# Kernel optimization log

Measured on AMD Instinct MI355X. Metric: run time of the kernel, lower is better.

## Reference

```python
import jax, jax.numpy as jnp
import numpy as np

KH, KW = 3, 3
STRIDE = 1
OUT_C = 512


def im2col(x, kh, kw, stride):
    # x: [N, C, H, W] -> col: [C*kh*kw, N*oh*ow]  (row order: C major, then kh, kw)
    N, C, H, W = x.shape
    oh = (H - kh) // stride + 1
    ow = (W - kw) // stride + 1
    rows = jnp.arange(oh)[:, None] * stride + jnp.arange(kh)[None, :]  # [oh, kh]
    cols = jnp.arange(ow)[:, None] * stride + jnp.arange(kw)[None, :]  # [ow, kw]
    # gather windows: result [N, C, oh, kh, ow, kw]
    A = x[:, :, rows[:, :, None, None], cols[None, None, :, :]]
    # permute to (C, kh, kw, N, oh, ow) then flatten, matching torch permute(1,4,5,0,2,3)
    col = jnp.transpose(A, (1, 3, 5, 0, 2, 4)).reshape(C * kh * kw, N * oh * ow)
    return col, oh, ow


def setup_inputs() -> dict:
    key = jax.random.key(0)
    k1, k2, k3 = jax.random.split(key, 3)
    N, C, H, W = 16, 256, 32, 32
    K_sel = (C * KH * KW) // 2  # 1152 rows kept by the binary mask
    x = jax.random.normal(k1, (N, C, H, W), dtype=jnp.float32)
    weight = jax.random.normal(k2, (K_sel, OUT_C), dtype=jnp.float32) * 0.02
    idx = jnp.sort(jax.random.randint(k3, (K_sel,), 0, C * KH * KW, dtype=jnp.int32))
    return {"x": x, "weight": weight, "idx": idx}


def reference(x, weight, idx):
    N = x.shape[0]
    col, oh, ow = im2col(x, KH, KW, STRIDE)          # [C*kh*kw, N*oh*ow]
    x_tile = col[idx, :].T                            # gather masked rows -> [N*oh*ow, K_sel]
    conv_out = x_tile @ weight                        # [N*oh*ow, out_c]
    conv_out = conv_out.reshape(N, oh * ow, OUT_C)
    conv_out = jnp.transpose(conv_out, (0, 2, 1)).reshape(N, OUT_C, oh, ow)
    return conv_out
```

## Files before the change

kernel.cpp:

```cpp
#include <hip/hip_runtime.h>
#include <stdint.h>

#define N_IMG   16
#define C_IN    256
#define H_IN    32
#define W_IN    32
#define OH      30
#define OW      30
#define K_SEL   1152
#define OUTC    512
#define RY_TOT  (N_IMG * OH)
#define M_HAT   (RY_TOT * 32)
#define X_ELEMS (N_IMG * C_IN * H_IN * W_IN)
#define OUT_SP  (OH * OW)
#define CHW     (C_IN * H_IN * W_IN)

#define TO      256
#define TM      64
#define NMT     (M_HAT / TM)
#define NOT     (OUTC / TO)
#define BSTR    40
#define KITER   (K_SEL / 32)

typedef float f32x4  __attribute__((ext_vector_type(4)));
typedef short bf16x8 __attribute__((ext_vector_type(8)));

__device__ __forceinline__ unsigned short f2bf(float f) {
    unsigned int u = __float_as_uint(f);
    u += 0x7FFFu + ((u >> 16) & 1u);
    return (unsigned short)(u >> 16);
}

__device__ __forceinline__ void gl_lds16(const void* g, void* lds) {
    __builtin_amdgcn_global_load_lds(
        (const __attribute__((address_space(1))) unsigned int*)g,
        (__attribute__((address_space(3))) unsigned int*)lds,
        16, 0, 0);
}

__global__ void prep_kernel(const int* __restrict__ idx, const float* __restrict__ w,
                            int* __restrict__ koff, unsigned short* __restrict__ wT) {
    __shared__ float tile[32][33];
    const int bx = blockIdx.x, by = blockIdx.y, t = threadIdx.x;

    if (by == 0) {
        int k = bx * 256 + t;
        if (k < K_SEL) {
            int v = idx[k];
            int c = v / 9, rem = v - c * 9;
            int i = rem / 3, j = rem - i * 3;
            koff[k] = c * (H_IN * W_IN) + i * W_IN + j;
        }
    }
    const int s0 = bx * 32, o0 = by * 32;
    const int oc = t & 31, sg = t >> 5;
#pragma unroll
    for (int i = 0; i < 4; ++i) {
        int sl = sg * 4 + i;
        tile[sl][oc] = w[(s0 + sl) * OUTC + o0 + oc];
    }
    __syncthreads();
    const int ol = t >> 3, sq = t & 7;
    unsigned int u0 = (unsigned int)f2bf(tile[sq * 4 + 0][ol]) |
                      ((unsigned int)f2bf(tile[sq * 4 + 1][ol]) << 16);
    unsigned int u1 = (unsigned int)f2bf(tile[sq * 4 + 2][ol]) |
                      ((unsigned int)f2bf(tile[sq * 4 + 3][ol]) << 16);
    uint2 pk; pk.x = u0; pk.y = u1;
    *reinterpret_cast<uint2*>(&wT[(size_t)(o0 + ol) * K_SEL + s0 + sq * 4]) = pk;
}

__global__ __launch_bounds__(256, 2)
void gemm_kernel(const unsigned short* __restrict__ wT, const float* __restrict__ x,
                 const int* __restrict__ koff, float* __restrict__ out) {
    __shared__ __align__(16) unsigned short As[2][TO * 32];
    __shared__ __align__(16) unsigned short Bs[2][TM * BSTR];
    __shared__ int koS[K_SEL];

    const int t    = threadIdx.x;
    const int wave = t >> 6;
    const int lane = t & 63;
    const int quad = lane >> 4;
    const int lo   = lane & 15;

    const int bid = blockIdx.x;
    const int mt  = bid % NMT;
    const int ot  = bid / NMT;
    const int oBase = ot * TO;
    const int mBase = mt * TM;

    for (int i = t; i < K_SEL; i += 256) koS[i] = koff[i];

    const int xw  = t & 31;
    const int xwc = min(xw, 29);
    int basex[2];
#pragma unroll
    for (int ry = 0; ry < 2; ++ry) {
        int ryg = mt * 2 + ry;
        int n = ryg / 30, y = ryg - n * 30;
        basex[ry] = n * CHW + y * W_IN + xwc;
    }

    const int kq4 = t >> 5;
    const int ks  = kq4 * 4;

    const int lrow = lane >> 2, csw = (lane & 3) ^ ((lrow >> 1) & 3);
    const unsigned short* wrow[4];
#pragma unroll
    for (int i = 0; i < 4; ++i)
        wrow[i] = wT + (size_t)(oBase + wave * 64 + i * 16 + lrow) * K_SEL + csw * 8;
    unsigned short* lA[2][4];
#pragma unroll
    for (int b = 0; b < 2; ++b)
#pragma unroll
        for (int i = 0; i < 4; ++i)
            lA[b][i] = &As[b][(wave * 64 + i * 16) * 32];

    const int aswz = quad ^ ((lo >> 1) & 3);
    const unsigned short* aB[2] = {
        &As[0][(wave * 64 + lo) * 32 + aswz * 8],
        &As[1][(wave * 64 + lo) * 32 + aswz * 8] };
    const unsigned short* bB[2] = {
        &Bs[0][lo * BSTR + quad * 8],
        &Bs[1][lo * BSTR + quad * 8] };
    unsigned short* bW[2] = {
        &Bs[0][xw * BSTR + ks],
        &Bs[1][xw * BSTR + ks] };

    __syncthreads();

    f32x4 acc[4][4] = {};
    float v[2][2][4];

    {
        int4 k4 = *(const int4*)&koS[ks];
#pragma unroll
        for (int ry = 0; ry < 2; ++ry)
#pragma unroll
            for (int j = 0; j < 4; ++j)
                v[0][ry][j] = x[basex[ry] + ((const int*)&k4)[j]];
    }
    asm volatile("s_waitcnt vmcnt(0)" ::: "memory");
#pragma unroll
    for (int ry = 0; ry < 2; ++ry) {
        unsigned int u0 = (unsigned int)f2bf(v[0][ry][0]) |
                          ((unsigned int)f2bf(v[0][ry][1]) << 16);
        unsigned int u1 = (unsigned int)f2bf(v[0][ry][2]) |
                          ((unsigned int)f2bf(v[0][ry][3]) << 16);
        uint2 pk; pk.x = u0; pk.y = u1;
        *reinterpret_cast<uint2*>(bW[0] + ry * 32 * BSTR) = pk;
    }
#pragma unroll
    for (int i = 0; i < 4; ++i) gl_lds16(wrow[i], lA[0][i]);
    {
        int4 k4 = *(const int4*)&koS[32 + ks];
#pragma unroll
        for (int ry = 0; ry < 2; ++ry)
#pragma unroll
            for (int j = 0; j < 4; ++j)
                v[1][ry][j] = x[basex[ry] + ((const int*)&k4)[j]];
    }
    asm volatile("s_waitcnt lgkmcnt(0)" ::: "memory");
    __builtin_amdgcn_s_barrier();

#pragma unroll 2
    for (int kt = 0; kt < KITER; ++kt) {
        const int p = kt & 1, q = p ^ 1;

        {
            const int k1 = (kt + 1 < KITER ? kt + 1 : KITER - 1) * 32;
#pragma unroll
            for (int i = 0; i < 4; ++i) gl_lds16(wrow[i] + k1, lA[q][i]);
        }
        {
            const int k2 = (kt + 2 < KITER ? kt + 2 : KITER - 1) * 32;
            int4 k4 = *(const int4*)&koS[k2 + ks];
#pragma unroll
            for (int ry = 0; ry < 2; ++ry)
#pragma unroll
                for (int j = 0; j < 4; ++j)
                    v[p][ry][j] = x[basex[ry] + ((const int*)&k4)[j]];
        }
        asm volatile("s_waitcnt vmcnt(12)" ::: "memory");
#pragma unroll
        for (int ry = 0; ry < 2; ++ry) {
            unsigned int u0 = (unsigned int)f2bf(v[q][ry][0]) |
                              ((unsigned int)f2bf(v[q][ry][1]) << 16);
            unsigned int u1 = (unsigned int)f2bf(v[q][ry][2]) |
                              ((unsigned int)f2bf(v[q][ry][3]) << 16);
            uint2 pk; pk.x = u0; pk.y = u1;
            *reinterpret_cast<uint2*>(bW[q] + ry * 32 * BSTR) = pk;
        }
        bf16x8 a[4], b[4];
#pragma unroll
        for (int ms = 0; ms < 4; ++ms)
            a[ms] = *(const bf16x8*)(aB[p] + ms * 16 * 32);
#pragma unroll
        for (int ns = 0; ns < 4; ++ns)
            b[ns] = *(const bf16x8*)(bB[p] + ns * 16 * BSTR);
#pragma unroll
        for (int ms = 0; ms < 4; ++ms)
#pragma unroll
            for (int ns = 0; ns < 4; ++ns)
                acc[ms][ns] = __builtin_amdgcn_mfma_f32_16x16x32_bf16(
                    a[ms], b[ns], acc[ms][ns], 0, 0, 0);
        asm volatile("s_waitcnt lgkmcnt(0)" ::: "memory");
        __builtin_amdgcn_s_barrier();
    }

#pragma unroll
    for (int ns = 0; ns < 4; ++ns) {
        const int mh  = mBase + ns * 16 + lo;
        const int xwe = mh & 31;
        const int ryg = mh >> 5;
        const int n = ryg / 30, y = ryg - n * 30;
        if (xwe < OW) {
            const size_t ob = (size_t)n * (OUTC * OUT_SP) + (size_t)y * OW + xwe;
#pragma unroll
            for (int ms = 0; ms < 4; ++ms) {
                const int o0 = oBase + wave * 64 + ms * 16 + quad * 4;
#pragma unroll
                for (int r = 0; r < 4; ++r)
                    out[ob + (size_t)(o0 + r) * OUT_SP] = acc[ms][ns][r];
            }
        }
    }
}

extern "C" void kernel_launch(void* const* d_in, const int* in_sizes, int n_in,
                              void* d_out, int out_size, void* d_ws, size_t ws_size,
                              hipStream_t stream) {
    const float* x   = (const float*)d_in[0];
    const float* w   = (const float*)d_in[1];
    const int*   idx = (const int*)d_in[2];
    float*       out = (float*)d_out;

    char* ws = (char*)d_ws;
    int*            koff = (int*)ws;
    unsigned short* wT   = (unsigned short*)(ws + 4608);

    prep_kernel<<<dim3(K_SEL / 32, OUTC / 32), dim3(256), 0, stream>>>(idx, w, koff, wT);
    gemm_kernel<<<dim3(NMT * NOT), dim3(256), 0, stream>>>(wT, x, koff, out);
}
```

Measured before the change: 114.3 us.

## Double K-step to 64 and single-buffer weight tile with register-staged prefetch

Doubles the K tile from 32 to 64, which halves the number of main-loop iterations and barriers. Each iteration now issues 8 async weight loads and 16 gathered activation loads. The weight tile in LDS becomes single-buffered: each wave reads its fragments into registers first, waits on LDS, then overwrites its own rows with the next tile. This is safe because each wave only touches its own rows. The swizzle is adapted to the 64-wide rows and the vmcnt waits are retuned, at the cost of more registers for activations and fragments, which could pressure occupancy at 2 blocks per CU.

```diff
diff --git a/kernel.cpp b/kernel.cpp
--- a/kernel.cpp
+++ b/kernel.cpp
@@ -19,8 +19,9 @@
 #define TM      64
 #define NMT     (M_HAT / TM)
 #define NOT     (OUTC / TO)
-#define BSTR    40
-#define KITER   (K_SEL / 32)
+#define BK      64
+#define BSTR    72
+#define KIT2    (K_SEL / BK)
 
 typedef float f32x4  __attribute__((ext_vector_type(4)));
 typedef short bf16x8 __attribute__((ext_vector_type(8)));
@@ -72,7 +73,7 @@
 __global__ __launch_bounds__(256, 2)
 void gemm_kernel(const unsigned short* __restrict__ wT, const float* __restrict__ x,
                  const int* __restrict__ koff, float* __restrict__ out) {
-    __shared__ __align__(16) unsigned short As[2][TO * 32];
+    __shared__ __align__(16) unsigned short As[TO * BK];
     __shared__ __align__(16) unsigned short Bs[2][TM * BSTR];
     __shared__ int koS[K_SEL];
 
@@ -100,25 +101,21 @@
         basex[ry] = n * CHW + y * W_IN + xwc;
     }
 
-    const int kq4 = t >> 5;
-    const int ks  = kq4 * 4;
-
-    const int lrow = lane >> 2, csw = (lane & 3) ^ ((lrow >> 1) & 3);
-    const unsigned short* wrow[4];
-#pragma unroll
-    for (int i = 0; i < 4; ++i)
-        wrow[i] = wT + (size_t)(oBase + wave * 64 + i * 16 + lrow) * K_SEL + csw * 8;
-    unsigned short* lA[2][4];
-#pragma unroll
-    for (int b = 0; b < 2; ++b)
-#pragma unroll
-        for (int i = 0; i < 4; ++i)
-            lA[b][i] = &As[b][(wave * 64 + i * 16) * 32];
-
-    const int aswz = quad ^ ((lo >> 1) & 3);
-    const unsigned short* aB[2] = {
-        &As[0][(wave * 64 + lo) * 32 + aswz * 8],
-        &As[1][(wave * 64 + lo) * 32 + aswz * 8] };
+    const int kq = t >> 5;
+    const int ks = kq * 8;
+
+    const int arow = lane >> 3, csw = (lane & 7) ^ arow;
+    const unsigned short* wrow[8];
+#pragma unroll
+    for (int i = 0; i < 8; ++i)
+        wrow[i] = wT + (size_t)(oBase + wave * 64 + i * 8 + arow) * K_SEL + csw * 8;
+    unsigned short* lA[8];
+#pragma unroll
+    for (int i = 0; i < 8; ++i)
+        lA[i] = &As[(wave * 64 + i * 8) * BK];
+
+    const int ac0 = (quad ^ (lo & 7)) * 8;
+    const unsigned short* aBase = &As[(wave * 64 + lo) * BK];
     const unsigned short* bB[2] = {
         &Bs[0][lo * BSTR + quad * 8],
         &Bs[1][lo * BSTR + quad * 8] };
@@ -129,83 +126,89 @@
     __syncthreads();
 
     f32x4 acc[4][4] = {};
-    float v[2][2][4];
-
-    {
-        int4 k4 = *(const int4*)&koS[ks];
-#pragma unroll
-        for (int ry = 0; ry < 2; ++ry)
-#pragma unroll
-            for (int j = 0; j < 4; ++j)
-                v[0][ry][j] = x[basex[ry] + ((const int*)&k4)[j]];
-    }
+    float v[2][2][8];
+
+#define GATHER(KT, SLOT) do {                                                  \
+    int4 k4a = *(const int4*)&koS[(KT) * BK + ks];                             \
+    int4 k4b = *(const int4*)&koS[(KT) * BK + ks + 4];                         \
+    _Pragma("unroll")                                                          \
+    for (int ry = 0; ry < 2; ++ry)                                             \
+        _Pragma("unroll")                                                      \
+        for (int j = 0; j < 4; ++j) {                                          \
+            v[SLOT][ry][j]     = x[basex[ry] + ((const int*)&k4a)[j]];         \
+            v[SLOT][ry][4 + j] = x[basex[ry] + ((const int*)&k4b)[j]];         \
+        }                                                                      \
+} while (0)
+
+#define PACK(SLOT, DST) do {                                                   \
+    _Pragma("unroll")                                                          \
+    for (int ry = 0; ry < 2; ++ry) {                                           \
+        uint2 pk0, pk1;                                                        \
+        pk0.x = (unsigned int)f2bf(v[SLOT][ry][0]) |                           \
+                ((unsigned int)f2bf(v[SLOT][ry][1]) << 16);                    \
+        pk0.y = (unsigned int)f2bf(v[SLOT][ry][2]) |                           \
+                ((unsigned int)f2bf(v[SLOT][ry][3]) << 16);                    \
+        pk1.x = (unsigned int)f2bf(v[SLOT][ry][4]) |                           \
+                ((unsigned int)f2bf(v[SLOT][ry][5]) << 16);                    \
+        pk1.y = (unsigned int)f2bf(v[SLOT][ry][6]) |                           \
+                ((unsigned int)f2bf(v[SLOT][ry][7]) << 16);                    \
+        *reinterpret_cast<uint2*>(bW[DST] + ry * 32 * BSTR)     = pk0;         \
+        *reinterpret_cast<uint2*>(bW[DST] + ry * 32 * BSTR + 4) = pk1;         \
+    }                                                                          \
+} while (0)
+
+    GATHER(0, 0);
     asm volatile("s_waitcnt vmcnt(0)" ::: "memory");
-#pragma unroll
-    for (int ry = 0; ry < 2; ++ry) {
-        unsigned int u0 = (unsigned int)f2bf(v[0][ry][0]) |
-                          ((unsigned int)f2bf(v[0][ry][1]) << 16);
-        unsigned int u1 = (unsigned int)f2bf(v[0][ry][2]) |
-                          ((unsigned int)f2bf(v[0][ry][3]) << 16);
-        uint2 pk; pk.x = u0; pk.y = u1;
-        *reinterpret_cast<uint2*>(bW[0] + ry * 32 * BSTR) = pk;
-    }
-#pragma unroll
-    for (int i = 0; i < 4; ++i) gl_lds16(wrow[i], lA[0][i]);
-    {
-        int4 k4 = *(const int4*)&koS[32 + ks];
-#pragma unroll
-        for (int ry = 0; ry < 2; ++ry)
-#pragma unroll
-            for (int j = 0; j < 4; ++j)
-                v[1][ry][j] = x[basex[ry] + ((const int*)&k4)[j]];
-    }
+    PACK(0, 0);
+#pragma unroll
+    for (int i = 0; i < 8; ++i) gl_lds16(wrow[i], lA[i]);
+    GATHER(1, 1);
     asm volatile("s_waitcnt lgkmcnt(0)" ::: "memory");
     __builtin_amdgcn_s_barrier();
 
-#pragma unroll 2
-    for (int kt = 0; kt < KITER; ++kt) {
+    for (int kt = 0; kt < KIT2; ++kt) {
         const int p = kt & 1, q = p ^ 1;
 
+        asm volatile("s_waitcnt vmcnt(16)" ::: "memory");
+        bf16x8 a[4][2], b[4][2];
+#pragma unroll
+        for (int ms = 0; ms < 4; ++ms) {
+            a[ms][0] = *(const bf16x8*)(aBase + ms * 16 * BK + ac0);
+            a[ms][1] = *(const bf16x8*)(aBase + ms * 16 * BK + (ac0 ^ 32));
+        }
+#pragma unroll
+        for (int ns = 0; ns < 4; ++ns) {
+            b[ns][0] = *(const bf16x8*)(bB[p] + ns * 16 * BSTR);
+            b[ns][1] = *(const bf16x8*)(bB[p] + ns * 16 * BSTR + 32);
+        }
+        asm volatile("s_waitcnt lgkmcnt(0)" ::: "memory");
+        __builtin_amdgcn_sched_barrier(0);
+
         {
-            const int k1 = (kt + 1 < KITER ? kt + 1 : KITER - 1) * 32;
-#pragma unroll
-            for (int i = 0; i < 4; ++i) gl_lds16(wrow[i] + k1, lA[q][i]);
-        }
-        {
-            const int k2 = (kt + 2 < KITER ? kt + 2 : KITER - 1) * 32;
-            int4 k4 = *(const int4*)&koS[k2 + ks];
-#pragma unroll
-            for (int ry = 0; ry < 2; ++ry)
-#pragma unroll
-                for (int j = 0; j < 4; ++j)
-                    v[p][ry][j] = x[basex[ry] + ((const int*)&k4)[j]];
-        }
-        asm volatile("s_waitcnt vmcnt(12)" ::: "memory");
-#pragma unroll
-        for (int ry = 0; ry < 2; ++ry) {
-            unsigned int u0 = (unsigned int)f2bf(v[q][ry][0]) |
-                              ((unsigned int)f2bf(v[q][ry][1]) << 16);
-            unsigned int u1 = (unsigned int)f2bf(v[q][ry][2]) |
-                              ((unsigned int)f2bf(v[q][ry][3]) << 16);
-            uint2 pk; pk.x = u0; pk.y = u1;
-            *reinterpret_cast<uint2*>(bW[q] + ry * 32 * BSTR) = pk;
-        }
-        bf16x8 a[4], b[4];
+            const int k1 = (kt + 1 < KIT2 ? kt + 1 : KIT2 - 1) * BK;
+#pragma unroll
+            for (int i = 0; i < 8; ++i) gl_lds16(wrow[i] + k1, lA[i]);
+        }
+        GATHER((kt + 2 < KIT2 ? kt + 2 : KIT2 - 1), p);
+
+        asm volatile("s_waitcnt vmcnt(24)" ::: "memory");
+        PACK(q, q);
+
 #pragma unroll
         for (int ms = 0; ms < 4; ++ms)
-            a[ms] = *(const bf16x8*)(aB[p] + ms * 16 * 32);
-#pragma unroll
-        for (int ns = 0; ns < 4; ++ns)
-            b[ns] = *(const bf16x8*)(bB[p] + ns * 16 * BSTR);
-#pragma unroll
-        for (int ms = 0; ms < 4; ++ms)
-#pragma unroll
-            for (int ns = 0; ns < 4; ++ns)
+#pragma unroll
+            for (int ns = 0; ns < 4; ++ns) {
                 acc[ms][ns] = __builtin_amdgcn_mfma_f32_16x16x32_bf16(
-                    a[ms], b[ns], acc[ms][ns], 0, 0, 0);
+                    a[ms][0], b[ns][0], acc[ms][ns], 0, 0, 0);
+                acc[ms][ns] = __builtin_amdgcn_mfma_f32_16x16x32_bf16(
+                    a[ms][1], b[ns][1], acc[ms][ns], 0, 0, 0);
+            }
+
         asm volatile("s_waitcnt lgkmcnt(0)" ::: "memory");
         __builtin_amdgcn_s_barrier();
     }
+#undef GATHER
+#undef PACK
 
 #pragma unroll
     for (int ns = 0; ns < 4; ++ns) {
```

Measured after the change: 130.8 us. 1.14x slower.

## Pre-swizzle weights into MFMA fragment order and load A directly to registers

Applied to the files above, without the earlier changes.

The prep kernel now writes the bf16 weights in a layout that matches the per-lane MFMA A-fragment order. The GEMM kernel then loads A straight from global memory into registers, double-buffered across k-steps, and no longer stages it in LDS. The output tile is halved from 256 to 128 channels and occupancy is raised to 4 blocks per CU, which reduces LDS use and doubles the grid. The cost is that the im2col gather of x is repeated for twice as many blocks, and A is re-read from global or L2 by each block with less reuse.

```diff
diff --git a/kernel.cpp b/kernel.cpp
--- a/kernel.cpp
+++ b/kernel.cpp
@@ -15,7 +15,7 @@
 #define OUT_SP  (OH * OW)
 #define CHW     (C_IN * H_IN * W_IN)
 
-#define TO      256
+#define TO      128
 #define TM      64
 #define NMT     (M_HAT / TM)
 #define NOT     (OUTC / TO)
@@ -31,15 +31,8 @@
     return (unsigned short)(u >> 16);
 }
 
-__device__ __forceinline__ void gl_lds16(const void* g, void* lds) {
-    __builtin_amdgcn_global_load_lds(
-        (const __attribute__((address_space(1))) unsigned int*)g,
-        (__attribute__((address_space(3))) unsigned int*)lds,
-        16, 0, 0);
-}
-
 __global__ void prep_kernel(const int* __restrict__ idx, const float* __restrict__ w,
-                            int* __restrict__ koff, unsigned short* __restrict__ wT) {
+                            int* __restrict__ koff, unsigned short* __restrict__ wTf) {
     __shared__ float tile[32][33];
     const int bx = blockIdx.x, by = blockIdx.y, t = threadIdx.x;
 
@@ -66,13 +59,15 @@
     unsigned int u1 = (unsigned int)f2bf(tile[sq * 4 + 2][ol]) |
                       ((unsigned int)f2bf(tile[sq * 4 + 3][ol]) << 16);
     uint2 pk; pk.x = u0; pk.y = u1;
-    *reinterpret_cast<uint2*>(&wT[(size_t)(o0 + ol) * K_SEL + s0 + sq * 4]) = pk;
-}
-
-__global__ __launch_bounds__(256, 2)
-void gemm_kernel(const unsigned short* __restrict__ wT, const float* __restrict__ x,
+    const size_t fi =
+        (((((size_t)(by >> 1) * KITER + bx) * 4 + ((by * 2 + (ol >> 4)) & 3)) * 64
+          + (sq >> 1) * 16 + (ol & 15)) * 8) + (sq & 1) * 4;
+    *reinterpret_cast<uint2*>(&wTf[fi]) = pk;
+}
+
+__global__ __launch_bounds__(256, 4)
+void gemm_kernel(const unsigned short* __restrict__ wTf, const float* __restrict__ x,
                  const int* __restrict__ koff, float* __restrict__ out) {
-    __shared__ __align__(16) unsigned short As[2][TO * 32];
     __shared__ __align__(16) unsigned short Bs[2][TM * BSTR];
     __shared__ int koS[K_SEL];
 
@@ -103,22 +98,11 @@
     const int kq4 = t >> 5;
     const int ks  = kq4 * 4;
 
-    const int lrow = lane >> 2, csw = (lane & 3) ^ ((lrow >> 1) & 3);
-    const unsigned short* wrow[4];
-#pragma unroll
-    for (int i = 0; i < 4; ++i)
-        wrow[i] = wT + (size_t)(oBase + wave * 64 + i * 16 + lrow) * K_SEL + csw * 8;
-    unsigned short* lA[2][4];
-#pragma unroll
-    for (int b = 0; b < 2; ++b)
-#pragma unroll
-        for (int i = 0; i < 4; ++i)
-            lA[b][i] = &As[b][(wave * 64 + i * 16) * 32];
-
-    const int aswz = quad ^ ((lo >> 1) & 3);
-    const unsigned short* aB[2] = {
-        &As[0][(wave * 64 + lo) * 32 + aswz * 8],
-        &As[1][(wave * 64 + lo) * 32 + aswz * 8] };
+    const int ow64 = ot * 2 + (wave >> 1);
+    const int idx0 = (wave * 2) & 3;
+    const unsigned short* aP =
+        wTf + ((size_t)ow64 * KITER * 4 + idx0) * 64 * 8 + (size_t)lane * 8;
+
     const unsigned short* bB[2] = {
         &Bs[0][lo * BSTR + quad * 8],
         &Bs[1][lo * BSTR + quad * 8] };
@@ -128,7 +112,8 @@
 
     __syncthreads();
 
-    f32x4 acc[4][4] = {};
+    f32x4 acc[2][4] = {};
+    bf16x8 aR[2][2];
     float v[2][2][4];
 
     {
@@ -150,7 +135,8 @@
         *reinterpret_cast<uint2*>(bW[0] + ry * 32 * BSTR) = pk;
     }
 #pragma unroll
-    for (int i = 0; i < 4; ++i) gl_lds16(wrow[i], lA[0][i]);
+    for (int ms = 0; ms < 2; ++ms)
+        aR[0][ms] = *(const bf16x8*)(aP + (size_t)(0 * 4 + ms) * 64 * 8);
     {
         int4 k4 = *(const int4*)&koS[32 + ks];
 #pragma unroll
@@ -166,10 +152,16 @@
     for (int kt = 0; kt < KITER; ++kt) {
         const int p = kt & 1, q = p ^ 1;
 
+        bf16x8 b[4];
+#pragma unroll
+        for (int ns = 0; ns < 4; ++ns)
+            b[ns] = *(const bf16x8*)(bB[p] + ns * 16 * BSTR);
+
         {
-            const int k1 = (kt + 1 < KITER ? kt + 1 : KITER - 1) * 32;
-#pragma unroll
-            for (int i = 0; i < 4; ++i) gl_lds16(wrow[i] + k1, lA[q][i]);
+            const int k1 = (kt + 1 < KITER ? kt + 1 : KITER - 1);
+#pragma unroll
+            for (int ms = 0; ms < 2; ++ms)
+                aR[q][ms] = *(const bf16x8*)(aP + (size_t)(k1 * 4 + ms) * 64 * 8);
         }
         {
             const int k2 = (kt + 2 < KITER ? kt + 2 : KITER - 1) * 32;
@@ -180,7 +172,9 @@
                 for (int j = 0; j < 4; ++j)
                     v[p][ry][j] = x[basex[ry] + ((const int*)&k4)[j]];
         }
-        asm volatile("s_waitcnt vmcnt(12)" ::: "memory");
+        asm volatile("s_waitcnt vmcnt(10)" ::: "memory");
+        asm volatile("s_waitcnt lgkmcnt(0)" ::: "memory");
+        __builtin_amdgcn_sched_barrier(0);
 #pragma unroll
         for (int ry = 0; ry < 2; ++ry) {
             unsigned int u0 = (unsigned int)f2bf(v[q][ry][0]) |
@@ -190,19 +184,12 @@
             uint2 pk; pk.x = u0; pk.y = u1;
             *reinterpret_cast<uint2*>(bW[q] + ry * 32 * BSTR) = pk;
         }
-        bf16x8 a[4], b[4];
-#pragma unroll
-        for (int ms = 0; ms < 4; ++ms)
-            a[ms] = *(const bf16x8*)(aB[p] + ms * 16 * 32);
-#pragma unroll
-        for (int ns = 0; ns < 4; ++ns)
-            b[ns] = *(const bf16x8*)(bB[p] + ns * 16 * BSTR);
-#pragma unroll
-        for (int ms = 0; ms < 4; ++ms)
+#pragma unroll
+        for (int ms = 0; ms < 2; ++ms)
 #pragma unroll
             for (int ns = 0; ns < 4; ++ns)
                 acc[ms][ns] = __builtin_amdgcn_mfma_f32_16x16x32_bf16(
-                    a[ms], b[ns], acc[ms][ns], 0, 0, 0);
+                    aR[p][ms], b[ns], acc[ms][ns], 0, 0, 0);
         asm volatile("s_waitcnt lgkmcnt(0)" ::: "memory");
         __builtin_amdgcn_s_barrier();
     }
@@ -216,8 +203,8 @@
         if (xwe < OW) {
             const size_t ob = (size_t)n * (OUTC * OUT_SP) + (size_t)y * OW + xwe;
 #pragma unroll
-            for (int ms = 0; ms < 4; ++ms) {
-                const int o0 = oBase + wave * 64 + ms * 16 + quad * 4;
+            for (int ms = 0; ms < 2; ++ms) {
+                const int o0 = oBase + wave * 32 + ms * 16 + quad * 4;
 #pragma unroll
                 for (int r = 0; r < 4; ++r)
                     out[ob + (size_t)(o0 + r) * OUT_SP] = acc[ms][ns][r];
@@ -236,8 +223,8 @@
 
     char* ws = (char*)d_ws;
     int*            koff = (int*)ws;
-    unsigned short* wT   = (unsigned short*)(ws + 4608);
-
-    prep_kernel<<<dim3(K_SEL / 32, OUTC / 32), dim3(256), 0, stream>>>(idx, w, koff, wT);
-    gemm_kernel<<<dim3(NMT * NOT), dim3(256), 0, stream>>>(wT, x, koff, out);
-}
+    unsigned short* wTf  = (unsigned short*)(ws + 4608);
+
+    prep_kernel<<<dim3(K_SEL / 32, OUTC / 32), dim3(256), 0, stream>>>(idx, w, koff, wTf);
+    gemm_kernel<<<dim3(NMT * NOT), dim3(256), 0, stream>>>(wTf, x, koff, out);
+}
```

New measurement: 104.1 us. -8.9%, faster.
